# Kernel tuning notes

Measured on AMD Instinct MI355X. Metric: run time of the kernel, lower is better.

## Reference

```python
import jax, jax.numpy as jnp
import numpy as np

B, S, L, D = 4, 8, 350, 768  # paragraphs, sentences/paragraph, padded pair length, hidden
P = B * S * (S - 1)          # number of ordered sentence pairs = 224

# pair p -> (z, j, k): same enumeration order as the torch nested loops
_IDX = np.array([(z, j, k) for z in range(B) for j in range(S) for k in range(S) if j != k])
# each pair contributes its first-sentence embedding to segment (z,j) and second to (z,k)
_SEG = np.stack([_IDX[:, 0] * S + _IDX[:, 1], _IDX[:, 0] * S + _IDX[:, 2]], axis=1).reshape(-1)  # [2P]


def setup_inputs() -> dict:
    key = jax.random.key(0)
    ks = jax.random.split(key, 8)
    sc = 0.02
    all_output = jax.random.normal(ks[0], (P, L, D), dtype=jnp.float32)
    first_sep = jax.random.randint(ks[1], (P,), 5, 150).astype(jnp.int32)           # > 1
    second_sep = (first_sep + jax.random.randint(ks[2], (P,), 5, 150)).astype(jnp.int32)  # > first_sep+1, < L
    W1 = jax.random.normal(ks[3], (D, D), dtype=jnp.float32) * sc
    b1 = jnp.zeros((D,), jnp.float32)
    v1 = jax.random.normal(ks[4], (D,), dtype=jnp.float32) * sc
    vb1 = jnp.zeros((), jnp.float32)
    W2 = jax.random.normal(ks[5], (D, D), dtype=jnp.float32) * sc
    b2 = jnp.zeros((D,), jnp.float32)
    v2 = jax.random.normal(ks[6], (D,), dtype=jnp.float32) * sc
    vb2 = jnp.zeros((), jnp.float32)
    return {"all_output": all_output, "first_sep": first_sep, "second_sep": second_sep,
            "W1": W1, "b1": b1, "v1": v1, "vb1": vb1,
            "W2": W2, "b2": b2, "v2": v2, "vb2": vb2}


def reference(all_output, first_sep, second_sep, W1, b1, v1, vb1, W2, b2, v2, vb2):
    # pair_embeddings = [CLS] token of every pair
    pair_embeddings = all_output[:, 0, :]  # [P, D]

    # ---- level one: masked attention pooling over word positions ----
    u = jnp.tanh(all_output @ W1 + b1)          # [P, L, D]
    scores = u @ v1 + vb1                       # [P, L]
    pos = jnp.arange(L)[None, :]                # [1, L]
    mask1 = (pos >= 1) & (pos < first_sep[:, None])                 # tokens 1..first_sep-1
    mask2 = (pos > first_sep[:, None]) & (pos < second_sep[:, None])  # first_sep+1..second_sep-1

    def pool(mask):
        s = jnp.where(mask, scores, -jnp.inf)
        w = jax.nn.softmax(s, axis=1)           # [P, L]
        return jnp.einsum('pl,pld->pd', w, all_output)

    e1 = pool(mask1)                            # [P, D] first-sentence embeddings
    e2 = pool(mask2)                            # [P, D] second-sentence embeddings
    emb = jnp.stack([e1, e2], axis=1).reshape(2 * P, D)  # [2P, D]

    # ---- level two: segment attention pooling per (paragraph, sentence) group ----
    seg = jnp.asarray(_SEG)                     # [2P] segment ids, num_segments = B*S
    u2 = jnp.tanh(emb @ W2 + b2)                # [2P, D]
    sc = u2 @ v2 + vb2                          # [2P]
    num_seg = B * S
    smax = jax.ops.segment_max(sc, seg, num_segments=num_seg)
    ex = jnp.exp(sc - smax[seg])
    denom = jax.ops.segment_sum(ex, seg, num_segments=num_seg)
    w = ex / denom[seg]                         # segment softmax weights
    out2 = jax.ops.segment_sum(w[:, None] * emb, seg, num_segments=num_seg).reshape(B, S, D)
    return (pair_embeddings, out2)
```

## Files before the change

### kernel.cpp

```cpp
#include <hip/hip_runtime.h>
#include <math.h>

#define LSEQ   350
#define DDIM   768
#define NPAIR  224
#define MROWS1 78400
#define NSLAB1 613
#define MAXSLAB 520

typedef short bf16x8 __attribute__((ext_vector_type(8)));
typedef float f32x4  __attribute__((ext_vector_type(4)));

typedef const unsigned int __attribute__((address_space(1)))* gas_ptr;
typedef unsigned int __attribute__((address_space(3)))* las_ptr;

__device__ __forceinline__ void gload_lds16(const void* g, void* l) {
  __builtin_amdgcn_global_load_lds((gas_ptr)g, (las_ptr)l, 16, 0, 0);
}

__device__ __forceinline__ unsigned short f2bf(float x) {
  unsigned int u = __float_as_uint(x);
  unsigned int r = (u + 0x7FFFu + ((u >> 16) & 1u)) >> 16;
  return (unsigned short)r;
}

__device__ __forceinline__ float tanh_fast(float x) {
  float e = __expf(2.f * x);
  return 1.f - 2.f / (e + 1.f);
}

#define PREP_WT 1152
#define PREP_ZB 402
__global__ __launch_bounds__(256) void k_prep(
    const float* __restrict__ W1, const float* __restrict__ W2,
    unsigned short* __restrict__ Wt1, unsigned short* __restrict__ Wt2,
    const int* __restrict__ ssep, int* __restrict__ off,
    unsigned int* __restrict__ zreg) {
  const int b = blockIdx.x;
  const int t = threadIdx.x;
  if (b < PREP_WT) {
    const float* W = (b >= 576) ? W2 : W1;
    unsigned short* Wt = (b >= 576) ? Wt2 : Wt1;
    const int r = (b >= 576) ? b - 576 : b;
    const int bk = (r % 24) * 32, bn = (r / 24) * 32;
    __shared__ float tile[32][33];
    const int tx = t & 31, ty = t >> 5;
#pragma unroll
    for (int i = 0; i < 32; i += 8)
      tile[ty + i][tx] = W[(size_t)(bk + ty + i) * DDIM + bn + tx];
    __syncthreads();
#pragma unroll
    for (int i = 0; i < 32; i += 8)
      Wt[(size_t)(bn + ty + i) * DDIM + bk + tx] = f2bf(tile[tx][ty + i]);
  } else if (b == PREP_WT) {
    __shared__ int buf[256];
    int v = (t < NPAIR) ? (ssep[t] - 1) : 0;
    buf[t] = v;
    __syncthreads();
#pragma unroll
    for (int d = 1; d < 256; d <<= 1) {
      int add = (t >= d) ? buf[t - d] : 0;
      __syncthreads();
      buf[t] += add;
      __syncthreads();
    }
    if (t < NPAIR) off[t] = buf[t] - v;
    if (t == NPAIR - 1) off[NPAIR] = buf[t];
  } else {
    const int i = b - PREP_WT - 1;
    *((uint4*)zreg + (size_t)i * 256 + t) = make_uint4(0u, 0u, 0u, 0u);
  }
}

__global__ __launch_bounds__(192) void k_conv(const float* __restrict__ X,
                                              const int* __restrict__ ssep,
                                              const int* __restrict__ off,
                                              unsigned short* __restrict__ Xbf) {
  const int p = blockIdx.x, tile = blockIdx.y, z = blockIdx.z;
  const int nrow = ssep[p] - 1;
  const int r0 = tile * 128 + z * 32;
  if (r0 >= nrow) return;
  const int t = threadIdx.x;
  const int half = t / 96;
  const int tt = t - half * 96;
  const int o = off[p];
  const int rmax = min(32, nrow - r0);
  const float* src = X + ((size_t)p * LSEQ + 1 + r0) * DDIM + tt * 8;
  unsigned short* dst = Xbf + (size_t)(o + r0) * DDIM + tt * 8;
#pragma unroll 4
  for (int r = half; r < rmax; r += 2) {
    const float* s = src + (size_t)r * DDIM;
    float4 x = *(const float4*)s;
    float4 y = *(const float4*)(s + 4);
    unsigned int ux = __float_as_uint(x.x) + 0x8000u;
    unsigned int uy = __float_as_uint(x.y) + 0x8000u;
    unsigned int uz = __float_as_uint(x.z) + 0x8000u;
    unsigned int uw = __float_as_uint(x.w) + 0x8000u;
    unsigned int vx = __float_as_uint(y.x) + 0x8000u;
    unsigned int vy = __float_as_uint(y.y) + 0x8000u;
    unsigned int vz = __float_as_uint(y.z) + 0x8000u;
    unsigned int vw = __float_as_uint(y.w) + 0x8000u;
    *(uint4*)(dst + (size_t)r * DDIM) =
        make_uint4(__builtin_amdgcn_perm(uy, ux, 0x07060302u),
                   __builtin_amdgcn_perm(uw, uz, 0x07060302u),
                   __builtin_amdgcn_perm(vy, vx, 0x07060302u),
                   __builtin_amdgcn_perm(vw, vz, 0x07060302u));
  }
}

__global__ __launch_bounds__(256, 4) void k_gemm_c(
    const unsigned short* __restrict__ Xbf, const unsigned short* __restrict__ Wt,
    const float* __restrict__ bias, const float* __restrict__ vv,
    const int* __restrict__ off, float* __restrict__ scores_c) {
  const int Mtotal = off[NPAIR];
  const int b = blockIdx.x;
  const int g = b / 48, r = b - g * 48;
  const int slab = g * 8 + (r & 7);
  const int nchunk = r >> 3;
  if (slab * 128 >= Mtotal) return;

  const size_t arow0 = (size_t)slab * 128;
  const int n0 = nchunk * 128;

  __shared__ unsigned short As[128 * 32];
  __shared__ unsigned short Bs[128 * 32];

  const int t = threadIdx.x;
  const int lane = t & 63, w = t >> 6;
  const int l15 = t & 15;
  const int quad = (t >> 4) & 3;
  const int wm = w >> 1, wn = w & 1;
  const int lrow = lane >> 2;
  const int lcol = (lane & 3) * 8;

  f32x4 acc[4][4];
#pragma unroll
  for (int mi = 0; mi < 4; ++mi)
#pragma unroll
    for (int ni = 0; ni < 4; ++ni)
#pragma unroll
      for (int q = 0; q < 4; ++q) acc[mi][ni][q] = 0.f;

  for (int k0 = 0; k0 < DDIM; k0 += 32) {
#pragma unroll
    for (int j = 0; j < 2; ++j) {
      int seg = w * 2 + j;
      gload_lds16(Xbf + (arow0 + seg * 16 + lrow) * DDIM + k0 + lcol, As + seg * 512);
      gload_lds16(Wt + (size_t)(n0 + seg * 16 + lrow) * DDIM + k0 + lcol, Bs + seg * 512);
    }
    __syncthreads();

    bf16x8 a[4], bfr[4];
#pragma unroll
    for (int mi = 0; mi < 4; ++mi)
      a[mi] = *(const bf16x8*)&As[(wm * 64 + mi * 16 + l15) * 32 + quad * 8];
#pragma unroll
    for (int ni = 0; ni < 4; ++ni)
      bfr[ni] = *(const bf16x8*)&Bs[(wn * 64 + ni * 16 + l15) * 32 + quad * 8];
#pragma unroll
    for (int mi = 0; mi < 4; ++mi)
#pragma unroll
      for (int ni = 0; ni < 4; ++ni)
        acc[mi][ni] = __builtin_amdgcn_mfma_f32_16x16x32_bf16(a[mi], bfr[ni], acc[mi][ni], 0, 0, 0);
    __syncthreads();
  }

  float vvv[4], bbv[4];
#pragma unroll
  for (int ni = 0; ni < 4; ++ni) {
    int n = n0 + wn * 64 + ni * 16 + l15;
    vvv[ni] = vv[n];
    bbv[ni] = bias[n];
  }
#pragma unroll
  for (int mi = 0; mi < 4; ++mi) {
#pragma unroll
    for (int reg = 0; reg < 4; ++reg) {
      float s = 0.f;
#pragma unroll
      for (int ni = 0; ni < 4; ++ni)
        s += tanh_fast(acc[mi][ni][reg] + bbv[ni]) * vvv[ni];
      s += __shfl_xor(s, 1);
      s += __shfl_xor(s, 2);
      s += __shfl_xor(s, 4);
      s += __shfl_xor(s, 8);
      if (l15 == mi * 4 + reg) {
        int row = (int)arow0 + wm * 64 + mi * 16 + quad * 4 + reg;
        if (row < Mtotal) atomicAdd(&scores_c[row], s);
      }
    }
  }
}

__global__ __launch_bounds__(256, 2) void k_gemm_score(
    const float* __restrict__ X, const unsigned short* __restrict__ Wt,
    const float* __restrict__ bias, const float* __restrict__ vv,
    float* __restrict__ outs, int Mrows, int swz) {
  int slab, nchunk;
  if (swz) {
    int b = blockIdx.x;
    int g = b / 48, r = b - g * 48;
    slab = g * 8 + (r & 7);
    nchunk = r >> 3;
    if (slab >= NSLAB1) return;
  } else {
    slab = blockIdx.y;
    nchunk = blockIdx.x;
  }
  const int row0 = slab * 128;
  const int n0 = nchunk * 128;

  __shared__ unsigned short As[128][40];
  __shared__ unsigned short Bs[128][40];

  const int t = threadIdx.x;
  const int l15 = t & 15;
  const int quad = (t >> 4) & 3;
  const int w = t >> 6;
  const int wm = w >> 1, wn = w & 1;
  const int ar = t >> 3;
  const int ac = (t & 7) * 4;
  const int br = t >> 2;
  const int bc = (t & 3) * 8;

  f32x4 acc[4][4];
#pragma unroll
  for (int mi = 0; mi < 4; ++mi)
#pragma unroll
    for (int ni = 0; ni < 4; ++ni)
#pragma unroll
      for (int q = 0; q < 4; ++q) acc[mi][ni][q] = 0.f;

  for (int k0 = 0; k0 < DDIM; k0 += 32) {
#pragma unroll
    for (int pass = 0; pass < 4; ++pass) {
      int rr = ar + pass * 32;
      int row = row0 + rr;
      float4 x = make_float4(0.f, 0.f, 0.f, 0.f);
      if (row < Mrows) x = *(const float4*)(X + (size_t)row * DDIM + k0 + ac);
      unsigned int ux = __float_as_uint(x.x) + 0x8000u;
      unsigned int uy = __float_as_uint(x.y) + 0x8000u;
      unsigned int uz = __float_as_uint(x.z) + 0x8000u;
      unsigned int uw = __float_as_uint(x.w) + 0x8000u;
      *(uint2*)&As[rr][ac] = make_uint2(__builtin_amdgcn_perm(uy, ux, 0x07060302u),
                                        __builtin_amdgcn_perm(uw, uz, 0x07060302u));
    }
#pragma unroll
    for (int pp = 0; pp < 2; ++pp) {
      int rr = br + pp * 64;
      *(uint4*)&Bs[rr][bc] = *(const uint4*)(Wt + (size_t)(n0 + rr) * DDIM + k0 + bc);
    }
    __syncthreads();

    bf16x8 a[4], bfr[4];
#pragma unroll
    for (int mi = 0; mi < 4; ++mi)
      a[mi] = *(const bf16x8*)&As[wm * 64 + mi * 16 + l15][quad * 8];
#pragma unroll
    for (int ni = 0; ni < 4; ++ni)
      bfr[ni] = *(const bf16x8*)&Bs[wn * 64 + ni * 16 + l15][quad * 8];
#pragma unroll
    for (int mi = 0; mi < 4; ++mi)
#pragma unroll
      for (int ni = 0; ni < 4; ++ni)
        acc[mi][ni] = __builtin_amdgcn_mfma_f32_16x16x32_bf16(a[mi], bfr[ni], acc[mi][ni], 0, 0, 0);
    __syncthreads();
  }

  float vvv[4], bbv[4];
#pragma unroll
  for (int ni = 0; ni < 4; ++ni) {
    int n = n0 + wn * 64 + ni * 16 + l15;
    vvv[ni] = vv[n];
    bbv[ni] = bias[n];
  }
#pragma unroll
  for (int mi = 0; mi < 4; ++mi) {
#pragma unroll
    for (int reg = 0; reg < 4; ++reg) {
      float s = 0.f;
#pragma unroll
      for (int ni = 0; ni < 4; ++ni)
        s += tanh_fast(acc[mi][ni][reg] + bbv[ni]) * vvv[ni];
      s += __shfl_xor(s, 1);
      s += __shfl_xor(s, 2);
      s += __shfl_xor(s, 4);
      s += __shfl_xor(s, 8);
      if (l15 == mi * 4 + reg) {
        int row = row0 + wm * 64 + mi * 16 + quad * 4 + reg;
        if (row < Mrows) atomicAdd(&outs[row], s);
      }
    }
  }
}

__device__ __forceinline__ float block_reduce(float v, bool is_max, float* redbuf) {
#pragma unroll
  for (int off = 1; off < 64; off <<= 1) {
    float o = __shfl_xor(v, off);
    v = is_max ? fmaxf(v, o) : (v + o);
  }
  int wv = threadIdx.x >> 6;
  if ((threadIdx.x & 63) == 0) redbuf[wv] = v;
  __syncthreads();
  float r = is_max ? fmaxf(fmaxf(redbuf[0], redbuf[1]), fmaxf(redbuf[2], redbuf[3]))
                   : (redbuf[0] + redbuf[1] + redbuf[2] + redbuf[3]);
  __syncthreads();
  return r;
}

__global__ __launch_bounds__(256) void k_pool3(
    const unsigned short* __restrict__ Xbf, const float* __restrict__ X,
    const float* __restrict__ scores_c, const int* __restrict__ fsep,
    const int* __restrict__ ssep, const int* __restrict__ off,
    float* __restrict__ emb, float* __restrict__ out) {
  const int p = blockIdx.x, c = blockIdx.y, t = threadIdx.x;
  const int fs = fsep[p], ss = ssep[p];
  const int o = off[p];
  __shared__ float sw1[LSEQ], sw2[LSEQ];
  __shared__ float redbuf[4];

  float m1p = -INFINITY, m2p = -INFINITY;
  for (int l = t; l < LSEQ; l += 256) {
    float s = (l >= 1 && l < ss) ? scores_c[o + l - 1] : 0.f;
    float s1 = (l >= 1 && l < fs) ? s : -INFINITY;
    float s2 = (l > fs && l < ss) ? s : -INFINITY;
    sw1[l] = s1; sw2[l] = s2;
    m1p = fmaxf(m1p, s1); m2p = fmaxf(m2p, s2);
  }
  __syncthreads();
  float m1 = block_reduce(m1p, true, redbuf);
  float m2 = block_reduce(m2p, true, redbuf);
  float d1p = 0.f, d2p = 0.f;
  for (int l = t; l < LSEQ; l += 256) {
    float e1v = __expf(sw1[l] - m1);
    float e2v = __expf(sw2[l] - m2);
    sw1[l] = e1v; sw2[l] = e2v;
    d1p += e1v; d2p += e2v;
  }
  __syncthreads();
  float inv1 = 1.f / block_reduce(d1p, false, redbuf);
  float inv2 = 1.f / block_reduce(d2p, false, redbuf);

  if (t < 192) {
    if (c == 0) {
      *(float4*)(out + (size_t)p * DDIM + t * 4) =
          *(const float4*)(X + (size_t)p * LSEQ * DDIM + t * 4);
    }

    const int nch = (ss + 2) >> 2;
    const int lo = 1 + c * nch;
    const int hi = min(ss, lo + nch);

    float A1[4] = {0.f, 0.f, 0.f, 0.f}, A2[4] = {0.f, 0.f, 0.f, 0.f};
    const unsigned short* xb = Xbf + (size_t)o * DDIM + t * 4;
#pragma unroll 4
    for (int l = lo; l < hi; ++l) {
      float wa = sw1[l] * inv1, wb = sw2[l] * inv2;
      uint2 xv = *(const uint2*)(xb + (size_t)(l - 1) * DDIM);
      float x0 = __uint_as_float((xv.x & 0xFFFFu) << 16);
      float x1 = __uint_as_float(xv.x & 0xFFFF0000u);
      float x2 = __uint_as_float((xv.y & 0xFFFFu) << 16);
      float x3 = __uint_as_float(xv.y & 0xFFFF0000u);
      A1[0] += wa * x0; A1[1] += wa * x1; A1[2] += wa * x2; A1[3] += wa * x3;
      A2[0] += wb * x0; A2[1] += wb * x1; A2[2] += wb * x2; A2[3] += wb * x3;
    }
    float* e1 = emb + (size_t)(2 * p) * DDIM + t * 4;
    float* e2 = emb + (size_t)(2 * p + 1) * DDIM + t * 4;
    atomicAdd(&e1[0], A1[0]); atomicAdd(&e1[1], A1[1]);
    atomicAdd(&e1[2], A1[2]); atomicAdd(&e1[3], A1[3]);
    atomicAdd(&e2[0], A2[0]); atomicAdd(&e2[1], A2[1]);
    atomicAdd(&e2[2], A2[2]); atomicAdd(&e2[3], A2[3]);
  }
}

__global__ __launch_bounds__(256) void k_w1t(const float* __restrict__ W,
                                             unsigned short* __restrict__ Wt) {
  __shared__ float tile[32][33];
  int bk = blockIdx.x * 32, bn = blockIdx.y * 32;
  int tx = threadIdx.x & 31, ty = threadIdx.x >> 5;
#pragma unroll
  for (int i = 0; i < 32; i += 8)
    tile[ty + i][tx] = W[(size_t)(bk + ty + i) * DDIM + bn + tx];
  __syncthreads();
#pragma unroll
  for (int i = 0; i < 32; i += 8)
    Wt[(size_t)(bn + ty + i) * DDIM + bk + tx] = f2bf(tile[tx][ty + i]);
}

__global__ __launch_bounds__(256) void k_pool(
    const float* __restrict__ X, const float* __restrict__ scores,
    const int* __restrict__ fsep, const int* __restrict__ ssep,
    float* __restrict__ emb, float* __restrict__ out) {
  const int p = blockIdx.x;
  const int c = blockIdx.y;
  const int t = threadIdx.x;
  const int fs = fsep[p], ss = ssep[p];
  __shared__ float sw1[LSEQ], sw2[LSEQ];
  __shared__ float redbuf[4];

  float m1p = -INFINITY, m2p = -INFINITY;
  for (int l = t; l < LSEQ; l += 256) {
    float s = scores[p * LSEQ + l];
    float s1 = (l >= 1 && l < fs) ? s : -INFINITY;
    float s2 = (l > fs && l < ss) ? s : -INFINITY;
    sw1[l] = s1; sw2[l] = s2;
    m1p = fmaxf(m1p, s1); m2p = fmaxf(m2p, s2);
  }
  __syncthreads();
  float m1 = block_reduce(m1p, true, redbuf);
  float m2 = block_reduce(m2p, true, redbuf);
  float d1p = 0.f, d2p = 0.f;
  for (int l = t; l < LSEQ; l += 256) {
    float e1v = __expf(sw1[l] - m1);
    float e2v = __expf(sw2[l] - m2);
    sw1[l] = e1v; sw2[l] = e2v;
    d1p += e1v; d2p += e2v;
  }
  __syncthreads();
  float inv1 = 1.f / block_reduce(d1p, false, redbuf);
  float inv2 = 1.f / block_reduce(d2p, false, redbuf);
  const float* base = X + (size_t)p * LSEQ * DDIM;
  if (c == 0) {
    float* po = out + (size_t)p * DDIM;
    po[t] = base[t]; po[t + 256] = base[t + 256]; po[t + 512] = base[t + 512];
  }
  if (t < 192) {
    float4 A1 = make_float4(0.f, 0.f, 0.f, 0.f);
    float4 A2 = make_float4(0.f, 0.f, 0.f, 0.f);
    for (int l = 1 + c; l < ss; l += 8) {
      float wa = sw1[l] * inv1, wb = sw2[l] * inv2;
      float4 x = *(const float4*)(base + (size_t)l * DDIM + 4 * t);
      A1.x += wa * x.x; A1.y += wa * x.y; A1.z += wa * x.z; A1.w += wa * x.w;
      A2.x += wb * x.x; A2.y += wb * x.y; A2.z += wb * x.z; A2.w += wb * x.w;
    }
    float* e1 = emb + (size_t)(2 * p) * DDIM + 4 * t;
    float* e2 = emb + (size_t)(2 * p + 1) * DDIM + 4 * t;
    atomicAdd(&e1[0], A1.x); atomicAdd(&e1[1], A1.y);
    atomicAdd(&e1[2], A1.z); atomicAdd(&e1[3], A1.w);
    atomicAdd(&e2[0], A2.x); atomicAdd(&e2[1], A2.y);
    atomicAdd(&e2[2], A2.z); atomicAdd(&e2[3], A2.w);
  }
}

__global__ __launch_bounds__(256) void k_segout(
    const float* __restrict__ emb, const float* __restrict__ sc,
    float* __restrict__ out2) {
  const int g = blockIdx.x;
  const int z = g >> 3, j = g & 7;
  const int t = threadIdx.x;
  int ee[14];
#pragma unroll
  for (int i = 0; i < 7; ++i) ee[i] = 2 * (z * 56 + j * 7 + i);
#pragma unroll
  for (int i = 0; i < 7; ++i) {
    int j2 = i + (i >= j ? 1 : 0);
    int kk = j - (j > j2 ? 1 : 0);
    ee[7 + i] = 2 * (z * 56 + j2 * 7 + kk) + 1;
  }
  float sv[14];
  float m = -INFINITY;
#pragma unroll
  for (int i = 0; i < 14; ++i) { sv[i] = sc[ee[i]]; m = fmaxf(m, sv[i]); }
  float den = 0.f;
#pragma unroll
  for (int i = 0; i < 14; ++i) { sv[i] = __expf(sv[i] - m); den += sv[i]; }
  float inv = 1.f / den;
  float a0 = 0.f, a1 = 0.f, a2 = 0.f;
#pragma unroll
  for (int i = 0; i < 14; ++i) {
    float wgt = sv[i] * inv;
    const float* er = emb + (size_t)ee[i] * DDIM;
    a0 += wgt * er[t]; a1 += wgt * er[t + 256]; a2 += wgt * er[t + 512];
  }
  out2[(size_t)g * DDIM + t] = a0;
  out2[(size_t)g * DDIM + t + 256] = a1;
  out2[(size_t)g * DDIM + t + 512] = a2;
}

extern "C" void kernel_launch(void* const* d_in, const int* in_sizes, int n_in,
                              void* d_out, int out_size, void* d_ws, size_t ws_size,
                              hipStream_t stream) {
  const float* X  = (const float*)d_in[0];
  const int* fs   = (const int*)d_in[1];
  const int* ss   = (const int*)d_in[2];
  const float* W1 = (const float*)d_in[3];
  const float* b1 = (const float*)d_in[4];
  const float* v1 = (const float*)d_in[5];
  const float* W2 = (const float*)d_in[7];
  const float* b2 = (const float*)d_in[8];
  const float* v2 = (const float*)d_in[9];
  float* out = (float*)d_out;

  char* ws = (char*)d_ws;
  const size_t XBF_ROWS = (size_t)MAXSLAB * 128 + 128;
  const size_t OFF_OFF  = XBF_ROWS * DDIM * 2;
  const size_t OFF_WT1  = OFF_OFF + 1024;
  const size_t OFF_WT2  = OFF_WT1 + 1179648;
  const size_t OFF_SCC  = OFF_WT2 + 1179648;
  const size_t OFF_SC2  = OFF_SCC + 266752;
  const size_t OFF_EMB  = OFF_SCC + 269312;
  const size_t ZBYTES   = (size_t)PREP_ZB * 4096;
  const size_t NEED     = OFF_SCC + ZBYTES + 256;

  if (ws_size >= NEED) {
    unsigned short* Xbf = (unsigned short*)ws;
    int*   off     = (int*)(ws + OFF_OFF);
    unsigned short* Wt1 = (unsigned short*)(ws + OFF_WT1);
    unsigned short* Wt2 = (unsigned short*)(ws + OFF_WT2);
    float* scores_c = (float*)(ws + OFF_SCC);
    float* sc       = (float*)(ws + OFF_SC2);
    float* emb      = (float*)(ws + OFF_EMB);

    k_prep<<<PREP_WT + 1 + PREP_ZB, 256, 0, stream>>>(
        W1, W2, Wt1, Wt2, ss, off, (unsigned int*)scores_c);
    k_conv<<<dim3(NPAIR, 3, 4), 192, 0, stream>>>(X, ss, off, Xbf);
    k_gemm_c<<<65 * 48, 256, 0, stream>>>(Xbf, Wt1, b1, v1, off, scores_c);
    k_pool3<<<dim3(NPAIR, 4), 256, 0, stream>>>(Xbf, X, scores_c, fs, ss, off, emb, out);
    k_gemm_score<<<dim3(6, 4), 256, 0, stream>>>(emb, Wt2, b2, v2, sc, 448, 0);
    k_segout<<<32, 256, 0, stream>>>(emb, sc, out + (size_t)NPAIR * DDIM);
  } else {
    unsigned short* Wt = (unsigned short*)ws;
    float* scores = (float*)(ws + 1179648);
    float* emb    = (float*)(ws + 1493248);
    float* sc     = scores;

    k_w1t<<<dim3(24, 24), 256, 0, stream>>>(W1, Wt);
    hipMemsetAsync(scores, 0, MROWS1 * sizeof(float), stream);
    hipMemsetAsync(emb, 0, 448 * DDIM * sizeof(float), stream);
    k_gemm_score<<<77 * 48, 256, 0, stream>>>(X, Wt, b1, v1, scores, MROWS1, 1);
    k_pool<<<dim3(NPAIR, 8), 256, 0, stream>>>(X, scores, fs, ss, emb, out);
    k_w1t<<<dim3(24, 24), 256, 0, stream>>>(W2, Wt);
    hipMemsetAsync(sc, 0, 448 * sizeof(float), stream);
    k_gemm_score<<<dim3(6, 4), 256, 0, stream>>>(emb, Wt, b2, v2, sc, 448, 0);
    k_segout<<<32, 256, 0, stream>>>(emb, sc, out + (size_t)NPAIR * DDIM);
  }
}
```

Before: 468.7 us.

## Fuse bf16 conversion into prep kernel and double GEMM K-tile to 64

```diff
diff --git a/kernel.cpp b/kernel.cpp
--- a/kernel.cpp
+++ b/kernel.cpp
@@ -29,19 +29,64 @@
   return 1.f - 2.f / (e + 1.f);
 }
 
+#define PREP_CV 2688
 #define PREP_WT 1152
 #define PREP_ZB 402
+#define PREP_SCAN (PREP_CV + PREP_WT)
 __global__ __launch_bounds__(256) void k_prep(
-    const float* __restrict__ W1, const float* __restrict__ W2,
-    unsigned short* __restrict__ Wt1, unsigned short* __restrict__ Wt2,
-    const int* __restrict__ ssep, int* __restrict__ off,
-    unsigned int* __restrict__ zreg) {
+    const float* __restrict__ X, const float* __restrict__ W1,
+    const float* __restrict__ W2, unsigned short* __restrict__ Wt1,
+    unsigned short* __restrict__ Wt2, const int* __restrict__ ssep,
+    int* __restrict__ off, unsigned int* __restrict__ zreg,
+    unsigned short* __restrict__ Xbf) {
   const int b = blockIdx.x;
   const int t = threadIdx.x;
-  if (b < PREP_WT) {
-    const float* W = (b >= 576) ? W2 : W1;
-    unsigned short* Wt = (b >= 576) ? Wt2 : Wt1;
-    const int r = (b >= 576) ? b - 576 : b;
+  if (b < PREP_CV) {
+    const int p = b / 12;
+    const int rem = b - p * 12;
+    const int nrow = ssep[p] - 1;
+    const int r0 = (rem >> 2) * 128 + (rem & 3) * 32;
+    if (r0 >= nrow) return;
+    __shared__ int sbuf[256];
+    sbuf[t] = (t < NPAIR && t < p) ? (ssep[t] - 1) : 0;
+    __syncthreads();
+#pragma unroll
+    for (int d = 128; d > 0; d >>= 1) {
+      if (t < d) sbuf[t] += sbuf[t + d];
+      __syncthreads();
+    }
+    const int o = sbuf[0];
+    if (t < 192) {
+      const int half = t / 96;
+      const int tt = t - half * 96;
+      const int rmax = min(32, nrow - r0);
+      const float* src = X + ((size_t)p * LSEQ + 1 + r0) * DDIM + tt * 8;
+      unsigned short* dst = Xbf + (size_t)(o + r0) * DDIM + tt * 8;
+#pragma unroll 4
+      for (int rr = half; rr < rmax; rr += 2) {
+        const float* s = src + (size_t)rr * DDIM;
+        float4 x = *(const float4*)s;
+        float4 y = *(const float4*)(s + 4);
+        unsigned int ux = __float_as_uint(x.x) + 0x8000u;
+        unsigned int uy = __float_as_uint(x.y) + 0x8000u;
+        unsigned int uz = __float_as_uint(x.z) + 0x8000u;
+        unsigned int uw = __float_as_uint(x.w) + 0x8000u;
+        unsigned int vx = __float_as_uint(y.x) + 0x8000u;
+        unsigned int vy = __float_as_uint(y.y) + 0x8000u;
+        unsigned int vz = __float_as_uint(y.z) + 0x8000u;
+        unsigned int vw = __float_as_uint(y.w) + 0x8000u;
+        *(uint4*)(dst + (size_t)rr * DDIM) =
+            make_uint4(__builtin_amdgcn_perm(uy, ux, 0x07060302u),
+                       __builtin_amdgcn_perm(uw, uz, 0x07060302u),
+                       __builtin_amdgcn_perm(vy, vx, 0x07060302u),
+                       __builtin_amdgcn_perm(vw, vz, 0x07060302u));
+      }
+    }
+  } else if (b < PREP_SCAN) {
+    const int br = b - PREP_CV;
+    const float* W = (br >= 576) ? W2 : W1;
+    unsigned short* Wt = (br >= 576) ? Wt2 : Wt1;
+    const int r = (br >= 576) ? br - 576 : br;
     const int bk = (r % 24) * 32, bn = (r / 24) * 32;
     __shared__ float tile[32][33];
     const int tx = t & 31, ty = t >> 5;
@@ -52,7 +97,7 @@
 #pragma unroll
     for (int i = 0; i < 32; i += 8)
       Wt[(size_t)(bn + ty + i) * DDIM + bk + tx] = f2bf(tile[tx][ty + i]);
-  } else if (b == PREP_WT) {
+  } else if (b == PREP_SCAN) {
     __shared__ int buf[256];
     int v = (t < NPAIR) ? (ssep[t] - 1) : 0;
     buf[t] = v;
@@ -67,44 +112,8 @@
     if (t < NPAIR) off[t] = buf[t] - v;
     if (t == NPAIR - 1) off[NPAIR] = buf[t];
   } else {
-    const int i = b - PREP_WT - 1;
+    const int i = b - PREP_SCAN - 1;
     *((uint4*)zreg + (size_t)i * 256 + t) = make_uint4(0u, 0u, 0u, 0u);
-  }
-}
-
-__global__ __launch_bounds__(192) void k_conv(const float* __restrict__ X,
-                                              const int* __restrict__ ssep,
-                                              const int* __restrict__ off,
-                                              unsigned short* __restrict__ Xbf) {
-  const int p = blockIdx.x, tile = blockIdx.y, z = blockIdx.z;
-  const int nrow = ssep[p] - 1;
-  const int r0 = tile * 128 + z * 32;
-  if (r0 >= nrow) return;
-  const int t = threadIdx.x;
-  const int half = t / 96;
-  const int tt = t - half * 96;
-  const int o = off[p];
-  const int rmax = min(32, nrow - r0);
-  const float* src = X + ((size_t)p * LSEQ + 1 + r0) * DDIM + tt * 8;
-  unsigned short* dst = Xbf + (size_t)(o + r0) * DDIM + tt * 8;
-#pragma unroll 4
-  for (int r = half; r < rmax; r += 2) {
-    const float* s = src + (size_t)r * DDIM;
-    float4 x = *(const float4*)s;
-    float4 y = *(const float4*)(s + 4);
-    unsigned int ux = __float_as_uint(x.x) + 0x8000u;
-    unsigned int uy = __float_as_uint(x.y) + 0x8000u;
-    unsigned int uz = __float_as_uint(x.z) + 0x8000u;
-    unsigned int uw = __float_as_uint(x.w) + 0x8000u;
-    unsigned int vx = __float_as_uint(y.x) + 0x8000u;
-    unsigned int vy = __float_as_uint(y.y) + 0x8000u;
-    unsigned int vz = __float_as_uint(y.z) + 0x8000u;
-    unsigned int vw = __float_as_uint(y.w) + 0x8000u;
-    *(uint4*)(dst + (size_t)r * DDIM) =
-        make_uint4(__builtin_amdgcn_perm(uy, ux, 0x07060302u),
-                   __builtin_amdgcn_perm(uw, uz, 0x07060302u),
-                   __builtin_amdgcn_perm(vy, vx, 0x07060302u),
-                   __builtin_amdgcn_perm(vw, vz, 0x07060302u));
   }
 }
 
@@ -122,16 +131,16 @@
   const size_t arow0 = (size_t)slab * 128;
   const int n0 = nchunk * 128;
 
-  __shared__ unsigned short As[128 * 32];
-  __shared__ unsigned short Bs[128 * 32];
+  __shared__ unsigned short As[128 * 64];
+  __shared__ unsigned short Bs[128 * 64];
 
   const int t = threadIdx.x;
   const int lane = t & 63, w = t >> 6;
   const int l15 = t & 15;
   const int quad = (t >> 4) & 3;
   const int wm = w >> 1, wn = w & 1;
-  const int lrow = lane >> 2;
-  const int lcol = (lane & 3) * 8;
+  const int lrow8 = lane >> 3;
+  const int lcol8 = (lane & 7) * 8;
 
   f32x4 acc[4][4];
 #pragma unroll
@@ -141,27 +150,30 @@
 #pragma unroll
       for (int q = 0; q < 4; ++q) acc[mi][ni][q] = 0.f;
 
-  for (int k0 = 0; k0 < DDIM; k0 += 32) {
-#pragma unroll
-    for (int j = 0; j < 2; ++j) {
-      int seg = w * 2 + j;
-      gload_lds16(Xbf + (arow0 + seg * 16 + lrow) * DDIM + k0 + lcol, As + seg * 512);
-      gload_lds16(Wt + (size_t)(n0 + seg * 16 + lrow) * DDIM + k0 + lcol, Bs + seg * 512);
-    }
-    __syncthreads();
-
-    bf16x8 a[4], bfr[4];
-#pragma unroll
-    for (int mi = 0; mi < 4; ++mi)
-      a[mi] = *(const bf16x8*)&As[(wm * 64 + mi * 16 + l15) * 32 + quad * 8];
-#pragma unroll
-    for (int ni = 0; ni < 4; ++ni)
-      bfr[ni] = *(const bf16x8*)&Bs[(wn * 64 + ni * 16 + l15) * 32 + quad * 8];
-#pragma unroll
-    for (int mi = 0; mi < 4; ++mi)
+  for (int k0 = 0; k0 < DDIM; k0 += 64) {
+#pragma unroll
+    for (int j = 0; j < 4; ++j) {
+      int seg = w * 4 + j;
+      gload_lds16(Xbf + (arow0 + seg * 8 + lrow8) * DDIM + k0 + lcol8, As + seg * 512);
+      gload_lds16(Wt + (size_t)(n0 + seg * 8 + lrow8) * DDIM + k0 + lcol8, Bs + seg * 512);
+    }
+    __syncthreads();
+
+#pragma unroll
+    for (int kk = 0; kk < 64; kk += 32) {
+      bf16x8 a[4], bfr[4];
+#pragma unroll
+      for (int mi = 0; mi < 4; ++mi)
+        a[mi] = *(const bf16x8*)&As[(wm * 64 + mi * 16 + l15) * 64 + kk + quad * 8];
 #pragma unroll
       for (int ni = 0; ni < 4; ++ni)
-        acc[mi][ni] = __builtin_amdgcn_mfma_f32_16x16x32_bf16(a[mi], bfr[ni], acc[mi][ni], 0, 0, 0);
+        bfr[ni] = *(const bf16x8*)&Bs[(wn * 64 + ni * 16 + l15) * 64 + kk + quad * 8];
+#pragma unroll
+      for (int mi = 0; mi < 4; ++mi)
+#pragma unroll
+        for (int ni = 0; ni < 4; ++ni)
+          acc[mi][ni] = __builtin_amdgcn_mfma_f32_16x16x32_bf16(a[mi], bfr[ni], acc[mi][ni], 0, 0, 0);
+    }
     __syncthreads();
   }
 
@@ -512,9 +524,8 @@
     float* sc       = (float*)(ws + OFF_SC2);
     float* emb      = (float*)(ws + OFF_EMB);
 
-    k_prep<<<PREP_WT + 1 + PREP_ZB, 256, 0, stream>>>(
-        W1, W2, Wt1, Wt2, ss, off, (unsigned int*)scores_c);
-    k_conv<<<dim3(NPAIR, 3, 4), 192, 0, stream>>>(X, ss, off, Xbf);
+    k_prep<<<PREP_SCAN + 1 + PREP_ZB, 256, 0, stream>>>(
+        X, W1, W2, Wt1, Wt2, ss, off, (unsigned int*)scores_c, Xbf);
     k_gemm_c<<<65 * 48, 256, 0, stream>>>(Xbf, Wt1, b1, v1, off, scores_c);
     k_pool3<<<dim3(NPAIR, 4), 256, 0, stream>>>(Xbf, X, scores_c, fs, ss, off, emb, out);
     k_gemm_score<<<dim3(6, 4), 256, 0, stream>>>(emb, Wt2, b2, v2, sc, 448, 0);
```

New measurement: 469.5 us. No clear change (+0.2%).
